# Performance work log

Hardware: AMD Instinct MI355X
Metric: run time of the kernel (lower is better)

## Reference

```python
import jax, jax.numpy as jnp
import numpy as np

D = 128  # feature_dim

def setup_inputs() -> dict:
    key = jax.random.key(0)
    ks = jax.random.split(key, 10)
    B, Sq, Skv = 32, 2048, 2048
    scale = 1.0 / np.sqrt(D)
    inp = {
        'smiles_features': jax.random.normal(ks[0], (B, Skv, D), jnp.float32),
        'image_features': jax.random.normal(ks[1], (B, Sq, D), jnp.float32),
        'Wv': jax.random.normal(ks[2], (D, D), jnp.float32) * scale,
        'bv': jnp.zeros((D,), jnp.float32),
        'Wk': jax.random.normal(ks[3], (D, D), jnp.float32) * scale,
        'bk': jnp.zeros((D,), jnp.float32),
        'Wq': jax.random.normal(ks[4], (D, D), jnp.float32) * scale,
        'bq': jnp.zeros((D,), jnp.float32),
        'Wd': jax.random.normal(ks[5], (D, D), jnp.float32) * scale,
        'bd': jnp.zeros((D,), jnp.float32),
    }
    return inp

def reference(smiles_features, image_features, Wv, bv, Wk, bk, Wq, bq, Wd, bd):
    # Linear layers: y = x @ W^T + b (torch convention)
    V = smiles_features @ Wv.T + bv          # [B, Skv, D]
    K = smiles_features @ Wk.T + bk          # [B, Skv, D]
    Q = image_features @ Wq.T + bq           # [B, Sq, D]
    # energy = Q K^T / sqrt(128) (hard-coded 128 in original)
    energy = jnp.einsum('bqd,bkd->bqk', Q, K) / jnp.sqrt(jnp.float32(128.0))
    attention = jax.nn.softmax(energy, axis=-1)
    fusion = jnp.einsum('bqk,bkd->bqd', attention, V)
    output = fusion @ Wd.T + bd
    return output
```

## Files before the change

kernel.cpp:

```cpp
#include <hip/hip_runtime.h>
#include <hip/hip_bf16.h>

typedef __attribute__((ext_vector_type(4))) float f32x4;
typedef __attribute__((ext_vector_type(16))) float f32x16;
typedef __attribute__((ext_vector_type(8))) short bf16x8;
typedef __attribute__((ext_vector_type(4))) unsigned int uint4v;
typedef __attribute__((ext_vector_type(2))) unsigned int uint2v;

#define MFMA16(a, b, c) __builtin_amdgcn_mfma_f32_16x16x32_bf16(a, b, c, 0, 0, 0)
#define MFMA32(a, b, c) __builtin_amdgcn_mfma_f32_32x32x16_bf16(a, b, c, 0, 0, 0)

__device__ __forceinline__ unsigned short f2bf(float f) {
  union { float f; unsigned u; } v; v.f = f;
  unsigned r = v.u + 0x7fffu + ((v.u >> 16) & 1u);
  return (unsigned short)(r >> 16);
}
__device__ __forceinline__ unsigned pack2(float a, float b) {
  union { __hip_bfloat162 h2; unsigned u; } cv;
  cv.h2 = __hip_bfloat162(__float2bfloat16(a), __float2bfloat16(b));
  return cv.u;
}

__device__ __forceinline__ void swap32(unsigned a, unsigned b, int hi,
                                       unsigned& ox, unsigned& oy) {
#if __has_builtin(__builtin_amdgcn_permlane32_swap)
  uint2v r = __builtin_amdgcn_permlane32_swap(a, b, false, false);
  ox = r[0]; oy = r[1];
#else
  unsigned sb = __shfl_xor(b, 32);
  unsigned sa = __shfl_xor(a, 32);
  ox = hi ? sb : a;
  oy = hi ? b : sa;
#endif
}

__global__ __launch_bounds__(256)
void proj_qkv_kernel(const float* __restrict__ image,
                     const float* __restrict__ Wq, const float* __restrict__ bq,
                     float qscale,
                     const float* __restrict__ smiles,
                     const float* __restrict__ Wk, const float* __restrict__ bk,
                     const float* __restrict__ Wv, const float* __restrict__ bv,
                     unsigned short* __restrict__ Qout,
                     unsigned short* __restrict__ Kout,
                     unsigned short* __restrict__ Vout)
{
  __shared__ __align__(16) unsigned short Ws[128][136];
  __shared__ __align__(16) unsigned short Xs[64][136];
  const int t = threadIdx.x;
  const int wid = t >> 6;
  const int lane = t & 63;
  const int ln = lane & 15, g = lane >> 4;
  const bool isQ = blockIdx.x < 1024;
  const long row0 = (long)(isQ ? blockIdx.x : blockIdx.x - 1024) * 64;
  const float* x = isQ ? image : smiles;

#pragma unroll
  for (int i = 0; i < 8; ++i) {
    int idx = (i * 256 + t) * 4;
    int r = idx >> 7, c = idx & 127;
    const float4 x4 = *reinterpret_cast<const float4*>(x + row0 * 128 + idx);
    ushort4 xb;
    xb.x = f2bf(x4.x); xb.y = f2bf(x4.y); xb.z = f2bf(x4.z); xb.w = f2bf(x4.w);
    *reinterpret_cast<ushort4*>(&Xs[r][c]) = xb;
  }

  const float* W1 = isQ ? Wq : Wk;
  const float* b1 = isQ ? bq : bk;
  float bz[8];
#pragma unroll
  for (int tt = 0; tt < 8; ++tt) bz[tt] = b1[tt * 16 + ln];

#pragma unroll
  for (int i = 0; i < 16; ++i) {
    int idx = (i * 256 + t) * 4;
    int r = idx >> 7, c = idx & 127;
    const float4 w4 = *reinterpret_cast<const float4*>(W1 + idx);
    ushort4 wb;
    wb.x = f2bf(w4.x); wb.y = f2bf(w4.y); wb.z = f2bf(w4.z); wb.w = f2bf(w4.w);
    *reinterpret_cast<ushort4*>(&Ws[r][c]) = wb;
  }
  __syncthreads();

  f32x4 acc[8];
#pragma unroll
  for (int tt = 0; tt < 8; ++tt) acc[tt] = (f32x4){0.f, 0.f, 0.f, 0.f};
#pragma unroll
  for (int c = 0; c < 4; ++c) {
    bf16x8 af = *reinterpret_cast<const bf16x8*>(&Xs[wid * 16 + ln][c * 32 + g * 8]);
#pragma unroll
    for (int tt = 0; tt < 8; ++tt) {
      bf16x8 bfr = *reinterpret_cast<const bf16x8*>(&Ws[tt * 16 + ln][c * 32 + g * 8]);
      acc[tt] = MFMA16(af, bfr, acc[tt]);
    }
  }

  if (isQ) {
#pragma unroll
    for (int tt = 0; tt < 8; ++tt)
#pragma unroll
      for (int r = 0; r < 4; ++r) {
        long row = row0 + wid * 16 + g * 4 + r;
        Qout[row * 128 + tt * 16 + ln] = f2bf((acc[tt][r] + bz[tt]) * qscale);
      }
    return;
  }

#pragma unroll
  for (int tt = 0; tt < 8; ++tt)
#pragma unroll
    for (int r = 0; r < 4; ++r) {
      long row = row0 + wid * 16 + g * 4 + r;
      Kout[row * 128 + tt * 16 + ln] = f2bf(acc[tt][r] + bz[tt]);
    }

  __syncthreads();
#pragma unroll
  for (int i = 0; i < 16; ++i) {
    int idx = (i * 256 + t) * 4;
    int r = idx >> 7, c = idx & 127;
    const float4 w4 = *reinterpret_cast<const float4*>(Wv + idx);
    ushort4 wb;
    wb.x = f2bf(w4.x); wb.y = f2bf(w4.y); wb.z = f2bf(w4.z); wb.w = f2bf(w4.w);
    *reinterpret_cast<ushort4*>(&Ws[r][c]) = wb;
  }
  __syncthreads();

  float bzv[8];
#pragma unroll
  for (int tt = 0; tt < 8; ++tt) bzv[tt] = bv[tt * 16 + ln];
#pragma unroll
  for (int tt = 0; tt < 8; ++tt) acc[tt] = (f32x4){0.f, 0.f, 0.f, 0.f};
#pragma unroll
  for (int c = 0; c < 4; ++c) {
    bf16x8 af = *reinterpret_cast<const bf16x8*>(&Xs[wid * 16 + ln][c * 32 + g * 8]);
#pragma unroll
    for (int tt = 0; tt < 8; ++tt) {
      bf16x8 bfr = *reinterpret_cast<const bf16x8*>(&Ws[tt * 16 + ln][c * 32 + g * 8]);
      acc[tt] = MFMA16(af, bfr, acc[tt]);
    }
  }
#pragma unroll
  for (int tt = 0; tt < 8; ++tt)
#pragma unroll
    for (int r = 0; r < 4; ++r) {
      long row = row0 + wid * 16 + g * 4 + r;
      long bb = row >> 11, rr = row & 2047;
      Vout[(bb * 128 + tt * 16 + ln) * 2048 + rr] = f2bf(acc[tt][r] + bzv[tt]);
    }
}

__global__ __launch_bounds__(256)
void attn_kernel(const unsigned short* __restrict__ Qg,
                 const unsigned short* __restrict__ Kg,
                 const unsigned short* __restrict__ Vtg,
                 const float* __restrict__ Wd,
                 const float* __restrict__ bd,
                 float* __restrict__ Out)
{
  __shared__ __align__(16) unsigned char smem[69632];
  auto Ks = reinterpret_cast<unsigned short (*)[32][136]>(smem);
  auto Vs = reinterpret_cast<unsigned short (*)[128][40]>(smem + 17408);

  const int t = threadIdx.x;
  const int lane = t & 63;
  const int q = lane & 31;
  const int hi = lane >> 5;
  const int wid = t >> 6;

  const int gbid = blockIdx.x;
  const int k_ = gbid >> 3, r_ = gbid & 7;
  const int b = r_ + 8 * (k_ >> 4);
  const int j = k_ & 15;
  const int q0 = j * 128 + wid * 32;

  const unsigned short* Qb = Qg + (long)b * 2048 * 128;
  const unsigned short* Kb = Kg + (long)b * 2048 * 128;
  const unsigned short* Vb = Vtg + (long)b * 128 * 2048;

  const int kr = t >> 4, kc = (t & 15) * 8;
  const int vc = t >> 2, ko = (t & 3) * 8;

  bf16x8 qf[8];
#pragma unroll
  for (int c = 0; c < 8; ++c)
    qf[c] = *reinterpret_cast<const bf16x8*>(
        Qb + (long)(q0 + q) * 128 + c * 16 + hi * 8);

  f32x16 o[4];
#pragma unroll
  for (int dc = 0; dc < 4; ++dc)
#pragma unroll
    for (int r = 0; r < 16; ++r) o[dc][r] = 0.f;
  float mrun = -1e30f;
  float lrun = 0.f;

  uint4v kreg0 = *reinterpret_cast<const uint4v*>(Kb + (long)kr * 128 + kc);
  uint4v kreg1 = *reinterpret_cast<const uint4v*>(Kb + (long)(kr + 16) * 128 + kc);
  uint4v vreg0 = *reinterpret_cast<const uint4v*>(Vb + (long)vc * 2048 + ko);
  uint4v vreg1 = *reinterpret_cast<const uint4v*>(Vb + (long)(vc + 64) * 2048 + ko);
  *reinterpret_cast<uint4v*>(&Ks[0][kr][kc]) = kreg0;
  *reinterpret_cast<uint4v*>(&Ks[0][kr + 16][kc]) = kreg1;
  *reinterpret_cast<uint4v*>(&Vs[0][vc][ko]) = vreg0;
  *reinterpret_cast<uint4v*>(&Vs[0][vc + 64][ko]) = vreg1;
  kreg0 = *reinterpret_cast<const uint4v*>(Kb + (long)(32 + kr) * 128 + kc);
  kreg1 = *reinterpret_cast<const uint4v*>(Kb + (long)(32 + kr + 16) * 128 + kc);
  vreg0 = *reinterpret_cast<const uint4v*>(Vb + (long)vc * 2048 + 32 + ko);
  vreg1 = *reinterpret_cast<const uint4v*>(Vb + (long)(vc + 64) * 2048 + 32 + ko);
  __syncthreads();

  for (int kt = 0; kt < 64; ++kt) {
    const int cur = kt & 1;

    if (kt < 63) {
      const int nb = cur ^ 1;
      *reinterpret_cast<uint4v*>(&Ks[nb][kr][kc]) = kreg0;
      *reinterpret_cast<uint4v*>(&Ks[nb][kr + 16][kc]) = kreg1;
      *reinterpret_cast<uint4v*>(&Vs[nb][vc][ko]) = vreg0;
      *reinterpret_cast<uint4v*>(&Vs[nb][vc + 64][ko]) = vreg1;
      if (kt < 62) {
        const int nv0 = (kt + 2) * 32;
        kreg0 = *reinterpret_cast<const uint4v*>(Kb + (long)(nv0 + kr) * 128 + kc);
        kreg1 = *reinterpret_cast<const uint4v*>(Kb + (long)(nv0 + kr + 16) * 128 + kc);
        vreg0 = *reinterpret_cast<const uint4v*>(Vb + (long)vc * 2048 + nv0 + ko);
        vreg1 = *reinterpret_cast<const uint4v*>(Vb + (long)(vc + 64) * 2048 + nv0 + ko);
      }
    }

    f32x16 st;
#pragma unroll
    for (int r = 0; r < 16; ++r) st[r] = 0.f;
    __builtin_amdgcn_s_setprio(1);
#pragma unroll
    for (int c = 0; c < 8; ++c) {
      bf16x8 kf = *reinterpret_cast<const bf16x8*>(&Ks[cur][q][c * 16 + hi * 8]);
      st = MFMA32(kf, qf[c], st);
    }
    __builtin_amdgcn_s_setprio(0);

    float tm = st[0];
#pragma unroll
    for (int r = 1; r < 16; ++r) tm = fmaxf(tm, st[r]);
    tm = fmaxf(tm, __shfl_xor(tm, 32));

    float mcur = mrun;
    if (!__all(tm <= mcur + 8.0f)) {
      float mnew = fmaxf(mcur, tm);
      float al = __builtin_amdgcn_exp2f(mcur - mnew);
      mrun = mnew;
      mcur = mnew;
      lrun *= al;
#pragma unroll
      for (int r = 0; r < 16; ++r) {
        float ar = __shfl(al, (r & 3) + 8 * (r >> 2) + 4 * hi);
#pragma unroll
        for (int dc = 0; dc < 4; ++dc) o[dc][r] *= ar;
      }
    }

    unsigned pk[8];
    float s[8];
#pragma unroll
    for (int j2 = 0; j2 < 8; ++j2) {
      float pa_ = __builtin_amdgcn_exp2f(st[2 * j2] - mcur);
      float pb_ = __builtin_amdgcn_exp2f(st[2 * j2 + 1] - mcur);
      s[j2] = pa_ + pb_;
      pk[j2] = pack2(pa_, pb_);
    }
#pragma unroll
    for (int j2 = 0; j2 < 4; ++j2) s[j2] += s[j2 + 4];
    lrun += (s[0] + s[1]) + (s[2] + s[3]);

    union { unsigned u[4]; bf16x8 v; } pa0, pa1;
    swap32(pk[0], pk[2], hi, pa0.u[0], pa0.u[2]);
    swap32(pk[1], pk[3], hi, pa0.u[1], pa0.u[3]);
    swap32(pk[4], pk[6], hi, pa1.u[0], pa1.u[2]);
    swap32(pk[5], pk[7], hi, pa1.u[1], pa1.u[3]);

    __builtin_amdgcn_s_setprio(1);
#pragma unroll
    for (int dc = 0; dc < 4; ++dc) {
      bf16x8 vf0 = *reinterpret_cast<const bf16x8*>(&Vs[cur][dc * 32 + q][hi * 8]);
      bf16x8 vf1 = *reinterpret_cast<const bf16x8*>(&Vs[cur][dc * 32 + q][16 + hi * 8]);
      o[dc] = MFMA32(pa0.v, vf0, o[dc]);
      o[dc] = MFMA32(pa1.v, vf1, o[dc]);
    }
    __builtin_amdgcn_s_setprio(0);

    __syncthreads();
  }

  auto Wds = reinterpret_cast<unsigned short (*)[136]>(smem);
  auto Os  = reinterpret_cast<unsigned short (*)[136]>(smem + 34816 + wid * 8704);

#pragma unroll
  for (int i = 0; i < 16; ++i) {
    int idx = (i * 256 + t) * 4;
    int r = idx >> 7, c = idx & 127;
    const float4 w4 = *reinterpret_cast<const float4*>(Wd + idx);
    ushort4 wb;
    wb.x = f2bf(w4.x); wb.y = f2bf(w4.y); wb.z = f2bf(w4.z); wb.w = f2bf(w4.w);
    *reinterpret_cast<ushort4*>(&Wds[r][c]) = wb;
  }

  float ltot = lrun + __shfl_xor(lrun, 32);
  float inv = 1.f / ltot;
#pragma unroll
  for (int r = 0; r < 16; ++r) {
    const int qr = (r & 3) + 8 * (r >> 2) + 4 * hi;
    float invr = __shfl(inv, qr);
#pragma unroll
    for (int dc = 0; dc < 4; ++dc)
      Os[qr][dc * 32 + q] = f2bf(o[dc][r] * invr);
  }
  __syncthreads();

  f32x16 o2[4];
#pragma unroll
  for (int cc = 0; cc < 4; ++cc)
#pragma unroll
    for (int r = 0; r < 16; ++r) o2[cc][r] = 0.f;
  __builtin_amdgcn_s_setprio(1);
#pragma unroll
  for (int c = 0; c < 8; ++c) {
    bf16x8 af = *reinterpret_cast<const bf16x8*>(&Os[q][c * 16 + hi * 8]);
#pragma unroll
    for (int cc = 0; cc < 4; ++cc) {
      bf16x8 bfr = *reinterpret_cast<const bf16x8*>(&Wds[cc * 32 + q][c * 16 + hi * 8]);
      o2[cc] = MFMA32(af, bfr, o2[cc]);
    }
  }
  __builtin_amdgcn_s_setprio(0);

  float bdv[4];
#pragma unroll
  for (int cc = 0; cc < 4; ++cc) bdv[cc] = bd[cc * 32 + q];

#pragma unroll
  for (int r = 0; r < 16; ++r) {
    const int qr = (r & 3) + 8 * (r >> 2) + 4 * hi;
    long row = (long)b * 2048 + q0 + qr;
#pragma unroll
    for (int cc = 0; cc < 4; ++cc)
      Out[row * 128 + cc * 32 + q] = o2[cc][r] + bdv[cc];
  }
}

extern "C" void kernel_launch(void* const* d_in, const int* in_sizes, int n_in,
                              void* d_out, int out_size, void* d_ws, size_t ws_size,
                              hipStream_t stream)
{
  (void)in_sizes; (void)n_in; (void)out_size; (void)ws_size;
  const float* smiles = (const float*)d_in[0];
  const float* image  = (const float*)d_in[1];
  const float* Wv = (const float*)d_in[2]; const float* bv = (const float*)d_in[3];
  const float* Wk = (const float*)d_in[4]; const float* bk = (const float*)d_in[5];
  const float* Wq = (const float*)d_in[6]; const float* bq = (const float*)d_in[7];
  const float* Wd = (const float*)d_in[8]; const float* bd = (const float*)d_in[9];

  unsigned short* Qw = (unsigned short*)d_ws;
  unsigned short* Kw = Qw + 8388608;
  unsigned short* Vw = Kw + 8388608;

  const float qscale = 1.4426950408889634f * 0.08838834764831845f;

  dim3 blk(256);
  proj_qkv_kernel<<<dim3(2048), blk, 0, stream>>>(image, Wq, bq, qscale,
                                                  smiles, Wk, bk, Wv, bv,
                                                  Qw, Kw, Vw);
  attn_kernel<<<dim3(512), blk, 0, stream>>>(Qw, Kw, Vw, Wd, bd, (float*)d_out);
}
```

Baseline: 118.6 us.

## Double attention block to 8 waves covering 256 query rows

The attention kernel now runs 512 threads per block, with each block covering 256 query rows instead of 128, and launches 256 blocks instead of 512. Each K/V tile loaded into shared memory is shared by twice as many waves, halving global K/V traffic per query, and each thread now loads one K row and one V row per tile. The costs are a larger LDS footprint per block, fewer blocks for the 256 CUs, and heavier barrier synchronisation across 8 waves.

```diff
diff --git a/kernel.cpp b/kernel.cpp
--- a/kernel.cpp
+++ b/kernel.cpp
@@ -150,7 +150,7 @@
     }
 }
 
-__global__ __launch_bounds__(256)
+__global__ __launch_bounds__(512)
 void attn_kernel(const unsigned short* __restrict__ Qg,
                  const unsigned short* __restrict__ Kg,
                  const unsigned short* __restrict__ Vtg,
@@ -158,7 +158,7 @@
                  const float* __restrict__ bd,
                  float* __restrict__ Out)
 {
-  __shared__ __align__(16) unsigned char smem[69632];
+  __shared__ __align__(16) unsigned char smem[104448];
   auto Ks = reinterpret_cast<unsigned short (*)[32][136]>(smem);
   auto Vs = reinterpret_cast<unsigned short (*)[128][40]>(smem + 17408);
 
@@ -170,9 +170,9 @@
 
   const int gbid = blockIdx.x;
   const int k_ = gbid >> 3, r_ = gbid & 7;
-  const int b = r_ + 8 * (k_ >> 4);
-  const int j = k_ & 15;
-  const int q0 = j * 128 + wid * 32;
+  const int b = r_ + 8 * (k_ >> 3);
+  const int j = k_ & 7;
+  const int q0 = j * 256 + wid * 32;
 
   const unsigned short* Qb = Qg + (long)b * 2048 * 128;
   const unsigned short* Kb = Kg + (long)b * 2048 * 128;
@@ -195,18 +195,12 @@
   float mrun = -1e30f;
   float lrun = 0.f;
 
-  uint4v kreg0 = *reinterpret_cast<const uint4v*>(Kb + (long)kr * 128 + kc);
-  uint4v kreg1 = *reinterpret_cast<const uint4v*>(Kb + (long)(kr + 16) * 128 + kc);
-  uint4v vreg0 = *reinterpret_cast<const uint4v*>(Vb + (long)vc * 2048 + ko);
-  uint4v vreg1 = *reinterpret_cast<const uint4v*>(Vb + (long)(vc + 64) * 2048 + ko);
-  *reinterpret_cast<uint4v*>(&Ks[0][kr][kc]) = kreg0;
-  *reinterpret_cast<uint4v*>(&Ks[0][kr + 16][kc]) = kreg1;
-  *reinterpret_cast<uint4v*>(&Vs[0][vc][ko]) = vreg0;
-  *reinterpret_cast<uint4v*>(&Vs[0][vc + 64][ko]) = vreg1;
-  kreg0 = *reinterpret_cast<const uint4v*>(Kb + (long)(32 + kr) * 128 + kc);
-  kreg1 = *reinterpret_cast<const uint4v*>(Kb + (long)(32 + kr + 16) * 128 + kc);
-  vreg0 = *reinterpret_cast<const uint4v*>(Vb + (long)vc * 2048 + 32 + ko);
-  vreg1 = *reinterpret_cast<const uint4v*>(Vb + (long)(vc + 64) * 2048 + 32 + ko);
+  uint4v kreg = *reinterpret_cast<const uint4v*>(Kb + (long)kr * 128 + kc);
+  uint4v vreg = *reinterpret_cast<const uint4v*>(Vb + (long)vc * 2048 + ko);
+  *reinterpret_cast<uint4v*>(&Ks[0][kr][kc]) = kreg;
+  *reinterpret_cast<uint4v*>(&Vs[0][vc][ko]) = vreg;
+  kreg = *reinterpret_cast<const uint4v*>(Kb + (long)(32 + kr) * 128 + kc);
+  vreg = *reinterpret_cast<const uint4v*>(Vb + (long)vc * 2048 + 32 + ko);
   __syncthreads();
 
   for (int kt = 0; kt < 64; ++kt) {
@@ -214,16 +208,12 @@
 
     if (kt < 63) {
       const int nb = cur ^ 1;
-      *reinterpret_cast<uint4v*>(&Ks[nb][kr][kc]) = kreg0;
-      *reinterpret_cast<uint4v*>(&Ks[nb][kr + 16][kc]) = kreg1;
-      *reinterpret_cast<uint4v*>(&Vs[nb][vc][ko]) = vreg0;
-      *reinterpret_cast<uint4v*>(&Vs[nb][vc + 64][ko]) = vreg1;
+      *reinterpret_cast<uint4v*>(&Ks[nb][kr][kc]) = kreg;
+      *reinterpret_cast<uint4v*>(&Vs[nb][vc][ko]) = vreg;
       if (kt < 62) {
         const int nv0 = (kt + 2) * 32;
-        kreg0 = *reinterpret_cast<const uint4v*>(Kb + (long)(nv0 + kr) * 128 + kc);
-        kreg1 = *reinterpret_cast<const uint4v*>(Kb + (long)(nv0 + kr + 16) * 128 + kc);
-        vreg0 = *reinterpret_cast<const uint4v*>(Vb + (long)vc * 2048 + nv0 + ko);
-        vreg1 = *reinterpret_cast<const uint4v*>(Vb + (long)(vc + 64) * 2048 + nv0 + ko);
+        kreg = *reinterpret_cast<const uint4v*>(Kb + (long)(nv0 + kr) * 128 + kc);
+        vreg = *reinterpret_cast<const uint4v*>(Vb + (long)vc * 2048 + nv0 + ko);
       }
     }
 
@@ -294,8 +284,8 @@
   auto Os  = reinterpret_cast<unsigned short (*)[136]>(smem + 34816 + wid * 8704);
 
 #pragma unroll
-  for (int i = 0; i < 16; ++i) {
-    int idx = (i * 256 + t) * 4;
+  for (int i = 0; i < 8; ++i) {
+    int idx = (i * 512 + t) * 4;
     int r = idx >> 7, c = idx & 127;
     const float4 w4 = *reinterpret_cast<const float4*>(Wd + idx);
     ushort4 wb;
@@ -364,9 +354,8 @@
 
   const float qscale = 1.4426950408889634f * 0.08838834764831845f;
 
-  dim3 blk(256);
-  proj_qkv_kernel<<<dim3(2048), blk, 0, stream>>>(image, Wq, bq, qscale,
-                                                  smiles, Wk, bk, Wv, bv,
-                                                  Qw, Kw, Vw);
-  attn_kernel<<<dim3(512), blk, 0, stream>>>(Qw, Kw, Vw, Wd, bd, (float*)d_out);
-}
+  proj_qkv_kernel<<<dim3(2048), dim3(256), 0, stream>>>(image, Wq, bq, qscale,
+                                                        smiles, Wk, bk, Wv, bv,
+                                                        Qw, Kw, Vw);
+  attn_kernel<<<dim3(256), dim3(512), 0, stream>>>(Qw, Kw, Vw, Wd, bd, (float*)d_out);
+}
```

After: 114.3 us. -3.6%, faster.
